# Kernel tuning notes

Measured on AMD Instinct MI355X. Metric: run time of the kernel, lower is better.

The kernel has to match this reference:

```python
import math
import jax, jax.numpy as jnp
import numpy as np

STREAMS = 4
DIM = 1024
M = 16                      # routing granularity
BUS = STREAMS * DIM         # 4096
C = BUS // M                # 256
SINK_ITERS = 10
SINK_TAU = 0.05
B, L = 4, 2048


def rms_norm(x, gamma):
    # F.normalize(x, dim=-1) * sqrt(dim) * (gamma + 1)
    norm = jnp.sqrt(jnp.sum(x * x, axis=-1, keepdims=True))
    x = x / jnp.maximum(norm, 1e-12)
    return x * jnp.sqrt(jnp.asarray(x.shape[-1], x.dtype)) * (gamma + 1.0)


def sinkhorn_log(logits, num_iters=SINK_ITERS, tau=SINK_TAU):
    n = logits.shape[-1]
    Z = logits / tau
    lm = -math.log(n)
    u = jnp.zeros(Z.shape[:-1], Z.dtype)
    v = jnp.zeros(Z.shape[:-2] + (n,), Z.dtype)
    def body(_, uv):
        u, v = uv
        u = lm - jax.nn.logsumexp(Z + v[..., None, :], axis=-1)
        v = lm - jax.nn.logsumexp(Z + u[..., None], axis=-2)
        return (u, v)
    u, v = jax.lax.fori_loop(0, num_iters, body, (u, v))
    return jnp.exp(Z + u[..., None] + v[..., None, :]) * n


def setup_inputs() -> dict:
    key = jax.random.key(0)
    ks = jax.random.split(key, 8)
    residuals = jax.random.normal(ks[0], (B * STREAMS, L, DIM), jnp.float32)
    branch_output = jax.random.normal(ks[1], (B, L, DIM), jnp.float32)
    gamma = jax.random.normal(ks[2], (BUS,), jnp.float32) * 0.02
    H_res_logits = jnp.full((M, M), -8.0, jnp.float32)
    H_res_logits = H_res_logits.at[jnp.arange(M), jnp.arange(M)].set(0.0)
    phi_res = jax.random.normal(ks[3], (BUS, M * M), jnp.float32) * 0.02
    H_pre_logits = jnp.full((STREAMS,), -8.0, jnp.float32).at[0].set(0.0)
    phi_pre = jax.random.normal(ks[4], (BUS, STREAMS), jnp.float32) * 0.02
    H_post_logits = jnp.zeros((STREAMS,), jnp.float32)
    phi_post = jax.random.normal(ks[5], (BUS, STREAMS), jnp.float32) * 0.02
    a = jnp.asarray(0.01, jnp.float32)
    return dict(residuals=residuals, branch_output=branch_output, gamma=gamma,
                H_res_logits=H_res_logits, phi_res=phi_res, alpha_res=a,
                H_pre_logits=H_pre_logits, phi_pre=phi_pre, alpha_pre=a,
                H_post_logits=H_post_logits, phi_post=phi_post, alpha_post=a)


def reference(residuals, branch_output, gamma, H_res_logits, phi_res, alpha_res,
              H_pre_logits, phi_pre, alpha_pre, H_post_logits, phi_post, alpha_post):
    # (b s) l d -> b l s d
    res = residuals.reshape(B, STREAMS, L, DIM).transpose(0, 2, 1, 3)
    bus = res.reshape(B, L, BUS)
    bus_n = rms_norm(bus, gamma)

    raw = (bus_n @ phi_res).reshape(B, L, M, M)
    S = sinkhorn_log(alpha_res * raw + H_res_logits)
    H_res = S  # no identity mix

    H_pre = jax.nn.softmax(alpha_pre * (bus_n @ phi_pre) + H_pre_logits, axis=-1)
    H_post = jax.nn.softmax(alpha_post * (bus_n @ phi_post) + H_post_logits, axis=-1)

    reshaped = res.reshape(B, L, M, C)
    mixed = jnp.einsum('blst,blsc->bltc', H_res, reshaped).reshape(B, L, STREAMS, DIM)

    branch_input = jnp.einsum('bls,blsd->bld', H_pre, res)

    # depth connection with given branch_output
    branch_to_streams = branch_output[..., None, :] * H_post[..., :, None]
    out = mixed + branch_to_streams            # (B, L, STREAMS, DIM)
    out = out.transpose(0, 2, 1, 3).reshape(B * STREAMS, L, DIM)
    return out, branch_input
```

## Files before the change

kernel.cpp:

```cpp
#include <hip/hip_runtime.h>
#include <hip/hip_bf16.h>
#include <math.h>

#define NSTREAM 4
#define DIM     1024
#define BUSW    4096
#define NTOK    8192
#define NPAD    288
#define KSPLIT  4
#define KCH     1024
#define BM      64
#define BK      32
#define OUT0    ((size_t)16 * 2048 * 1024)

typedef short bf16x8 __attribute__((ext_vector_type(8)));
typedef float f32x4  __attribute__((ext_vector_type(4)));

__device__ __forceinline__ unsigned short f2bf(float f) {
    union { float f; unsigned int u; } x; x.f = f;
    unsigned int r = x.u + 0x7fffu + ((x.u >> 16) & 1u);
    return (unsigned short)(r >> 16);
}
__device__ __forceinline__ unsigned int pack2(float a, float b) {
    return (unsigned int)f2bf(a) | ((unsigned int)f2bf(b) << 16);
}

__device__ __forceinline__ void gload_lds16(const void* g, void* l) {
    __builtin_amdgcn_global_load_lds(
        (const __attribute__((address_space(1))) unsigned int*)g,
        (__attribute__((address_space(3))) unsigned int*)l, 16, 0, 0);
}

__global__ void prep_w_kernel(const float* __restrict__ gamma,
                              const float* __restrict__ phi_res,
                              const float* __restrict__ phi_pre,
                              const float* __restrict__ phi_post,
                              unsigned short* __restrict__ W) {
    int idx = blockIdx.x * 256 + threadIdx.x;
    int n = idx >> 12;
    int k = idx & 4095;
    float v = 0.0f;
    if (n < 256)      v = phi_res[k * 256 + n];
    else if (n < 260) v = phi_pre[k * 4 + (n - 256)];
    else if (n < 264) v = phi_post[k * 4 + (n - 260)];
    v *= (gamma[k] + 1.0f);
    W[idx] = f2bf(v);
}

__launch_bounds__(256, 3)
__global__ void gemm_raw_kernel(const float* __restrict__ residuals,
                                const unsigned short* __restrict__ W,
                                float* __restrict__ raw_part) {
    __shared__ __align__(16) unsigned short Alds[2][BM * BK];
    __shared__ __align__(16) unsigned short Blds[2][NPAD * BK];

    const int tid = threadIdx.x;
    const int wid = tid >> 6, lane = tid & 63;
    const int tb = blockIdx.x, kc = blockIdx.y;
    const int row0 = tb * BM;

    f32x4 acc[2][9];
#pragma unroll
    for (int i = 0; i < 2; i++)
#pragma unroll
        for (int j = 0; j < 9; j++) acc[i][j] = (f32x4){0.f, 0.f, 0.f, 0.f};

    const int arow = tid >> 2;
    const int aj   = tid & 3;
    const int tok  = row0 + arow;
    const int bidx = tok >> 11, lidx = tok & 2047;
    const float* abase = residuals +
        (((size_t)(bidx * 4 + kc) * 2048 + lidx) * 1024 + aj * 8);
    const int asl = (arow * 4 + (aj ^ ((arow >> 1) & 3))) * 8;

    const char* wbytes = (const char*)(W + (size_t)kc * KCH);
    const char* bsrc[5];
    int bdo[5];
    bool bok[5];
#pragma unroll
    for (int i = 0; i < 5; i++) {
        int idx = i * 256 + tid;
        bok[i] = idx < (NPAD * BK) / 8;
        int rn = idx >> 2, js = idx & 3;
        int jg = js ^ ((rn >> 1) & 3);
        bsrc[i] = wbytes + (size_t)rn * (BUSW * 2) + jg * 16;
        bdo[i] = idx * 16;
    }

    const int fr = lane & 15, hf = lane >> 4;
    const int wr = (wid >> 1) * 32;
    const int wc = (wid & 1) * 144;

    int aoff[2], boff[9];
#pragma unroll
    for (int mt = 0; mt < 2; mt++) {
        int row = wr + mt * 16 + fr;
        aoff[mt] = (row * 4 + (hf ^ ((row >> 1) & 3))) * 8;
    }
#pragma unroll
    for (int nt = 0; nt < 9; nt++) {
        int row = wc + nt * 16 + fr;
        boff[nt] = (row * 4 + (hf ^ ((row >> 1) & 3))) * 8;
    }

    float4 fa0, fa1;

#pragma unroll
    for (int i = 0; i < 5; i++)
        if (bok[i]) gload_lds16(bsrc[i], (char*)Blds[0] + bdo[i]);
    fa0 = *(const float4*)abase;
    fa1 = *(const float4*)(abase + 4);
    {
        uint4 ua;
        ua.x = pack2(fa0.x, fa0.y); ua.y = pack2(fa0.z, fa0.w);
        ua.z = pack2(fa1.x, fa1.y); ua.w = pack2(fa1.z, fa1.w);
        *(uint4*)&Alds[0][asl] = ua;
    }
    __syncthreads();

    auto step = [&](int kt, int cb, int nb) {
        if (kt < KCH / BK - 1) {
#pragma unroll
            for (int i = 0; i < 5; i++)
                if (bok[i])
                    gload_lds16(bsrc[i] + (size_t)(kt + 1) * (BK * 2),
                                (char*)Blds[nb] + bdo[i]);
            const float* ap = abase + (kt + 1) * BK;
            fa0 = *(const float4*)ap;
            fa1 = *(const float4*)(ap + 4);
        }
        bf16x8 afrag[2];
#pragma unroll
        for (int mt = 0; mt < 2; mt++)
            afrag[mt] = *(const bf16x8*)&Alds[cb][aoff[mt]];
#pragma unroll
        for (int nt = 0; nt < 9; nt++) {
            bf16x8 bfrag = *(const bf16x8*)&Blds[cb][boff[nt]];
            acc[0][nt] = __builtin_amdgcn_mfma_f32_16x16x32_bf16(
                afrag[0], bfrag, acc[0][nt], 0, 0, 0);
            acc[1][nt] = __builtin_amdgcn_mfma_f32_16x16x32_bf16(
                afrag[1], bfrag, acc[1][nt], 0, 0, 0);
        }
        if (kt < KCH / BK - 1) {
            uint4 ua;
            ua.x = pack2(fa0.x, fa0.y); ua.y = pack2(fa0.z, fa0.w);
            ua.z = pack2(fa1.x, fa1.y); ua.w = pack2(fa1.z, fa1.w);
            *(uint4*)&Alds[nb][asl] = ua;
            __syncthreads();
        }
    };

#pragma unroll 1
    for (int kt = 0; kt < KCH / BK; kt += 2) {
        step(kt,     0, 1);
        step(kt + 1, 1, 0);
    }

#pragma unroll
    for (int mt = 0; mt < 2; mt++)
#pragma unroll
        for (int nt = 0; nt < 9; nt++)
#pragma unroll
            for (int r = 0; r < 4; r++) {
                int token = row0 + wr + mt * 16 + hf * 4 + r;
                int col   = wc + nt * 16 + fr;
                raw_part[((size_t)kc * NTOK + token) * NPAD + col] = acc[mt][nt][r];
            }
}

__global__ void fused_tail_kernel(const float* __restrict__ residuals,
                                  const float* __restrict__ branch_output,
                                  const float* __restrict__ H_res_logits,
                                  const float* __restrict__ alpha_res_p,
                                  const float* __restrict__ H_pre_logits,
                                  const float* __restrict__ alpha_pre_p,
                                  const float* __restrict__ H_post_logits,
                                  const float* __restrict__ alpha_post_p,
                                  const float* __restrict__ raw_part,
                                  float* __restrict__ out) {
    const int t = blockIdx.x;
    const int b = t >> 11, l = t & 2047;
    const int tid = threadIdx.x;
    const int wid = tid >> 6, lane = tid & 63;

    __shared__ float Zl[256];
    __shared__ float au[16], bv[16];
    __shared__ float extra[8];
    __shared__ float hpre[4], hpost[4];
    __shared__ float redbuf[4];

    float rsum = 0.f;
#pragma unroll
    for (int kc = 0; kc < 4; kc++)
        rsum += raw_part[((size_t)kc * NTOK + t) * NPAD + tid];
    float esum = 0.f;
    if (tid < 8) {
#pragma unroll
        for (int kc = 0; kc < 4; kc++)
            esum += raw_part[((size_t)kc * NTOK + t) * NPAD + 256 + tid];
    }

    const float* rbase = residuals + ((size_t)b * 4 * 2048 + l) * 1024;
    float busr[16];
    float sumsq = 0.f;
#pragma unroll
    for (int j = 0; j < 16; j++) {
        busr[j] = rbase[(size_t)(j >> 2) * 2048 * 1024 + (j & 3) * 256 + tid];
        sumsq += busr[j] * busr[j];
    }
#pragma unroll
    for (int off = 32; off > 0; off >>= 1) sumsq += __shfl_down(sumsq, off, 64);
    if (lane == 0) redbuf[wid] = sumsq;
    __syncthreads();

    const float ss = redbuf[0] + redbuf[1] + redbuf[2] + redbuf[3];
    const float scale = 64.0f / fmaxf(sqrtf(ss), 1e-12f);

    const float a_res = alpha_res_p[0];
    Zl[tid] = __expf((a_res * scale * rsum + H_res_logits[tid]) * 20.0f);
    if (tid < 8) extra[tid] = esum;

    const float* bo = branch_output + ((size_t)b * 2048 + l) * 1024;
    float bor[4];
#pragma unroll
    for (int j = 0; j < 4; j++) bor[j] = bo[j * 256 + tid];

    __syncthreads();

    if (wid == 0) {
        const float c0 = 1.0f / 16.0f;
        const bool act = lane < 16;
        const int r = lane & 15;
        if (act) bv[r] = 1.0f;
        __builtin_amdgcn_sched_barrier(0);
        float a_own = 0.f;
        for (int it = 0; it < 10; it++) {
            if (act) {
                float s2 = 0.f;
#pragma unroll
                for (int c = 0; c < 16; c++) s2 += Zl[r * 16 + c] * bv[c];
                a_own = c0 / s2;
                au[r] = a_own;
            }
            __builtin_amdgcn_sched_barrier(0);
            if (act) {
                float s2 = 0.f;
#pragma unroll
                for (int rr = 0; rr < 16; rr++) s2 += Zl[rr * 16 + r] * au[rr];
                bv[r] = c0 / s2;
            }
            __builtin_amdgcn_sched_barrier(0);
        }
        if (act) {
#pragma unroll
            for (int c = 0; c < 16; c++)
                Zl[r * 16 + c] = 16.0f * Zl[r * 16 + c] * a_own * bv[c];
        }
    } else if (wid == 1) {
        if (lane < 8) {
            const int s = lane & 3;
            const bool pre = lane < 4;
            const float alpha = pre ? alpha_pre_p[0] : alpha_post_p[0];
            const float logit = pre ? H_pre_logits[s] : H_post_logits[s];
            float pv = alpha * scale * extra[pre ? s : 4 + s] + logit;
            float pm = fmaxf(pv, __shfl_xor(pv, 1, 4));
            pm = fmaxf(pm, __shfl_xor(pm, 2, 4));
            float e = __expf(pv - pm);
            float s2 = e + __shfl_xor(e, 1, 4);
            s2 += __shfl_xor(s2, 2, 4);
            float h = e / s2;
            if (pre) hpre[s] = h; else hpost[s] = h;
        }
    }
    __syncthreads();

#pragma unroll
    for (int tc = 0; tc < 16; tc++) {
        float acc2 = 0.f;
#pragma unroll
        for (int s = 0; s < 16; s++) acc2 += Zl[s * 16 + tc] * busr[s];
        int sout = tc >> 2, d = (tc & 3) * 256 + tid;
        float val = acc2 + bor[tc & 3] * hpost[sout];
        out[((size_t)(b * 4 + sout) * 2048 + l) * 1024 + d] = val;
    }

#pragma unroll
    for (int q = 0; q < 4; q++) {
        float bi = 0.f;
#pragma unroll
        for (int s = 0; s < 4; s++) bi += hpre[s] * busr[s * 4 + q];
        out[OUT0 + ((size_t)b * 2048 + l) * 1024 + q * 256 + tid] = bi;
    }
}

extern "C" void kernel_launch(void* const* d_in, const int* in_sizes, int n_in,
                              void* d_out, int out_size, void* d_ws, size_t ws_size,
                              hipStream_t stream) {
    const float* residuals  = (const float*)d_in[0];
    const float* branch_out = (const float*)d_in[1];
    const float* gamma      = (const float*)d_in[2];
    const float* H_res_log  = (const float*)d_in[3];
    const float* phi_res    = (const float*)d_in[4];
    const float* alpha_res  = (const float*)d_in[5];
    const float* H_pre_log  = (const float*)d_in[6];
    const float* phi_pre    = (const float*)d_in[7];
    const float* alpha_pre  = (const float*)d_in[8];
    const float* H_post_log = (const float*)d_in[9];
    const float* phi_post   = (const float*)d_in[10];
    const float* alpha_post = (const float*)d_in[11];

    unsigned short* W = (unsigned short*)d_ws;
    float* raw_part = (float*)((char*)d_ws + (size_t)NPAD * BUSW * 2);
    float* out = (float*)d_out;

    hipLaunchKernelGGL(prep_w_kernel, dim3(NPAD * BUSW / 256), dim3(256), 0, stream,
                       gamma, phi_res, phi_pre, phi_post, W);
    hipLaunchKernelGGL(gemm_raw_kernel, dim3(NTOK / BM, KSPLIT), dim3(256), 0, stream,
                       residuals, W, raw_part);
    hipLaunchKernelGGL(fused_tail_kernel, dim3(NTOK), dim3(256), 0, stream,
                       residuals, branch_out, H_res_log, alpha_res,
                       H_pre_log, alpha_pre, H_post_log, alpha_post, raw_part, out);
}
```

Baseline: 386.8 us.

## Collapse fused tail kernel to a single wavefront per token

The tail kernel now runs one 64-lane wavefront per token instead of four, so each lane holds 64 bus values and 16 branch values in registers. The sum-of-squares reduction becomes a wave-level xor shuffle, and every __syncthreads is replaced by sched barriers, which removes block-level synchronisation and the idle waves that used to sit through the serial Sinkhorn loop. In exchange, register pressure per lane rises sharply and each wave issues more loads and stores on its own, which could lower occupancy or memory-level parallelism.

```diff
diff --git a/kernel.cpp b/kernel.cpp
--- a/kernel.cpp
+++ b/kernel.cpp
@@ -168,6 +168,7 @@
             }
 }
 
+__launch_bounds__(64, 4)
 __global__ void fused_tail_kernel(const float* __restrict__ residuals,
                                   const float* __restrict__ branch_output,
                                   const float* __restrict__ H_res_logits,
@@ -180,54 +181,77 @@
                                   float* __restrict__ out) {
     const int t = blockIdx.x;
     const int b = t >> 11, l = t & 2047;
-    const int tid = threadIdx.x;
-    const int wid = tid >> 6, lane = tid & 63;
+    const int lane = threadIdx.x;
 
     __shared__ float Zl[256];
     __shared__ float au[16], bv[16];
-    __shared__ float extra[8];
     __shared__ float hpre[4], hpost[4];
-    __shared__ float redbuf[4];
-
-    float rsum = 0.f;
-#pragma unroll
-    for (int kc = 0; kc < 4; kc++)
-        rsum += raw_part[((size_t)kc * NTOK + t) * NPAD + tid];
+
+    float rs[4];
+#pragma unroll
+    for (int j = 0; j < 4; j++) {
+        float v = 0.f;
+#pragma unroll
+        for (int kc = 0; kc < 4; kc++)
+            v += raw_part[((size_t)kc * NTOK + t) * NPAD + j * 64 + lane];
+        rs[j] = v;
+    }
     float esum = 0.f;
-    if (tid < 8) {
+    if (lane < 8) {
 #pragma unroll
         for (int kc = 0; kc < 4; kc++)
-            esum += raw_part[((size_t)kc * NTOK + t) * NPAD + 256 + tid];
+            esum += raw_part[((size_t)kc * NTOK + t) * NPAD + 256 + lane];
     }
 
     const float* rbase = residuals + ((size_t)b * 4 * 2048 + l) * 1024;
-    float busr[16];
+    float busr[64];
     float sumsq = 0.f;
 #pragma unroll
-    for (int j = 0; j < 16; j++) {
-        busr[j] = rbase[(size_t)(j >> 2) * 2048 * 1024 + (j & 3) * 256 + tid];
-        sumsq += busr[j] * busr[j];
-    }
-#pragma unroll
-    for (int off = 32; off > 0; off >>= 1) sumsq += __shfl_down(sumsq, off, 64);
-    if (lane == 0) redbuf[wid] = sumsq;
-    __syncthreads();
-
-    const float ss = redbuf[0] + redbuf[1] + redbuf[2] + redbuf[3];
-    const float scale = 64.0f / fmaxf(sqrtf(ss), 1e-12f);
+    for (int s = 0; s < 16; s++)
+#pragma unroll
+        for (int c4 = 0; c4 < 4; c4++) {
+            float v = rbase[(size_t)(s >> 2) * 2048 * 1024
+                            + (s & 3) * 256 + c4 * 64 + lane];
+            busr[s * 4 + c4] = v;
+            sumsq += v * v;
+        }
+
+    const float* bo = branch_output + ((size_t)b * 2048 + l) * 1024;
+    float bor[16];
+#pragma unroll
+    for (int q = 0; q < 4; q++)
+#pragma unroll
+        for (int c4 = 0; c4 < 4; c4++)
+            bor[q * 4 + c4] = bo[q * 256 + c4 * 64 + lane];
+
+#pragma unroll
+    for (int off = 32; off > 0; off >>= 1) sumsq += __shfl_xor(sumsq, off, 64);
+    const float scale = 64.0f / fmaxf(sqrtf(sumsq), 1e-12f);
 
     const float a_res = alpha_res_p[0];
-    Zl[tid] = __expf((a_res * scale * rsum + H_res_logits[tid]) * 20.0f);
-    if (tid < 8) extra[tid] = esum;
-
-    const float* bo = branch_output + ((size_t)b * 2048 + l) * 1024;
-    float bor[4];
-#pragma unroll
-    for (int j = 0; j < 4; j++) bor[j] = bo[j * 256 + tid];
-
-    __syncthreads();
-
-    if (wid == 0) {
+#pragma unroll
+    for (int j = 0; j < 4; j++) {
+        int m = j * 64 + lane;
+        Zl[m] = __expf((a_res * scale * rs[j] + H_res_logits[m]) * 20.0f);
+    }
+
+    if (lane < 8) {
+        const int s = lane & 3;
+        const bool pre = lane < 4;
+        const float alpha = pre ? alpha_pre_p[0] : alpha_post_p[0];
+        const float logit = pre ? H_pre_logits[s] : H_post_logits[s];
+        float pv = alpha * scale * esum + logit;
+        float pm = fmaxf(pv, __shfl_xor(pv, 1, 4));
+        pm = fmaxf(pm, __shfl_xor(pm, 2, 4));
+        float e = __expf(pv - pm);
+        float s2 = e + __shfl_xor(e, 1, 4);
+        s2 += __shfl_xor(s2, 2, 4);
+        float h = e / s2;
+        if (pre) hpre[s] = h; else hpost[s] = h;
+    }
+    __builtin_amdgcn_sched_barrier(0);
+
+    {
         const float c0 = 1.0f / 16.0f;
         const bool act = lane < 16;
         const int r = lane & 15;
@@ -256,41 +280,38 @@
             for (int c = 0; c < 16; c++)
                 Zl[r * 16 + c] = 16.0f * Zl[r * 16 + c] * a_own * bv[c];
         }
-    } else if (wid == 1) {
-        if (lane < 8) {
-            const int s = lane & 3;
-            const bool pre = lane < 4;
-            const float alpha = pre ? alpha_pre_p[0] : alpha_post_p[0];
-            const float logit = pre ? H_pre_logits[s] : H_post_logits[s];
-            float pv = alpha * scale * extra[pre ? s : 4 + s] + logit;
-            float pm = fmaxf(pv, __shfl_xor(pv, 1, 4));
-            pm = fmaxf(pm, __shfl_xor(pm, 2, 4));
-            float e = __expf(pv - pm);
-            float s2 = e + __shfl_xor(e, 1, 4);
-            s2 += __shfl_xor(s2, 2, 4);
-            float h = e / s2;
-            if (pre) hpre[s] = h; else hpost[s] = h;
-        }
-    }
-    __syncthreads();
+        __builtin_amdgcn_sched_barrier(0);
+    }
 
 #pragma unroll
     for (int tc = 0; tc < 16; tc++) {
-        float acc2 = 0.f;
-#pragma unroll
-        for (int s = 0; s < 16; s++) acc2 += Zl[s * 16 + tc] * busr[s];
-        int sout = tc >> 2, d = (tc & 3) * 256 + tid;
-        float val = acc2 + bor[tc & 3] * hpost[sout];
-        out[((size_t)(b * 4 + sout) * 2048 + l) * 1024 + d] = val;
-    }
-
-#pragma unroll
-    for (int q = 0; q < 4; q++) {
-        float bi = 0.f;
-#pragma unroll
-        for (int s = 0; s < 4; s++) bi += hpre[s] * busr[s * 4 + q];
-        out[OUT0 + ((size_t)b * 2048 + l) * 1024 + q * 256 + tid] = bi;
-    }
+        float Srow[16];
+#pragma unroll
+        for (int s = 0; s < 16; s++) Srow[s] = Zl[s * 16 + tc];
+        const int sout = tc >> 2;
+        const float hp = hpost[sout];
+#pragma unroll
+        for (int c4 = 0; c4 < 4; c4++) {
+            float acc2 = 0.f;
+#pragma unroll
+            for (int s = 0; s < 16; s++) acc2 += Srow[s] * busr[s * 4 + c4];
+            int d = (tc & 3) * 256 + c4 * 64 + lane;
+            out[((size_t)(b * 4 + sout) * 2048 + l) * 1024 + d]
+                = acc2 + bor[(tc & 3) * 4 + c4] * hp;
+        }
+    }
+
+    const float hp0 = hpre[0], hp1 = hpre[1], hp2 = hpre[2], hp3 = hpre[3];
+#pragma unroll
+    for (int q = 0; q < 4; q++)
+#pragma unroll
+        for (int c4 = 0; c4 < 4; c4++) {
+            float bi = hp0 * busr[(0 * 4 + q) * 4 + c4]
+                     + hp1 * busr[(1 * 4 + q) * 4 + c4]
+                     + hp2 * busr[(2 * 4 + q) * 4 + c4]
+                     + hp3 * busr[(3 * 4 + q) * 4 + c4];
+            out[OUT0 + ((size_t)b * 2048 + l) * 1024 + q * 256 + c4 * 64 + lane] = bi;
+        }
 }
 
 extern "C" void kernel_launch(void* const* d_in, const int* in_sizes, int n_in,
@@ -317,7 +338,7 @@
                        gamma, phi_res, phi_pre, phi_post, W);
     hipLaunchKernelGGL(gemm_raw_kernel, dim3(NTOK / BM, KSPLIT), dim3(256), 0, stream,
                        residuals, W, raw_part);
-    hipLaunchKernelGGL(fused_tail_kernel, dim3(NTOK), dim3(256), 0, stream,
+    hipLaunchKernelGGL(fused_tail_kernel, dim3(NTOK), dim3(64), 0, stream,
                        residuals, branch_out, H_res_log, alpha_res,
                        H_pre_log, alpha_pre, H_post_log, alpha_post, raw_part, out);
 }
```

After: 448.1 us. 15.8% more time.
